# Kernel tuning notes

Measured on AMD Instinct MI355X. Metric: run time of the kernel, lower is better.

The kernel has to match this reference:

```python
import jax, jax.numpy as jnp
import numpy as np

E, D_IN, D_HID, D_OUT, B = 8, 128, 256, 128, 65536


def setup_inputs() -> dict:
    key = jax.random.key(0)
    ks = jax.random.split(key, 6)
    s1 = 1.0 / np.sqrt(D_IN)
    s2 = 1.0 / np.sqrt(D_HID)
    return {
        "x": jax.random.normal(ks[0], (B, D_IN), dtype=jnp.float32),
        "weights": jax.random.uniform(ks[1], (B, E), dtype=jnp.float32),
        "W1": jax.random.uniform(ks[2], (E, D_IN, D_HID), jnp.float32, -s1, s1),
        "b1": jax.random.uniform(ks[3], (E, D_HID), jnp.float32, -s1, s1),
        "W2": jax.random.uniform(ks[4], (E, D_HID, D_OUT), jnp.float32, -s2, s2),
        "b2": jax.random.uniform(ks[5], (E, D_OUT), jnp.float32, -s2, s2),
    }


def reference(x, weights, W1, b1, W2, b2):
    # all-experts dense MLP: every expert processes the full batch
    h = jax.nn.relu(jnp.einsum("bi,eih->beh", x, W1) + b1[None])  # [B,E,H]
    y = jnp.einsum("beh,eho->beo", h, W2) + b2[None]              # [B,E,O]
    # weighted combine over experts
    return jnp.einsum("beo,be->bo", y, weights)                   # [B,O]
```

## Files before the change

### kernel.cpp

```cpp
#include <hip/hip_runtime.h>


#define E_    8
#define DIN_  128
#define DH_   256
#define DOUT_ 128
#define BM_   128
#define NCHUNK 32
#define REC1  20480

typedef __attribute__((ext_vector_type(8))) short bf16x8;
typedef __attribute__((ext_vector_type(16))) float f32x16;
typedef __attribute__((ext_vector_type(2))) unsigned int uint2v;

__device__ __forceinline__ unsigned short f2bf(float f) {
  union { float f; unsigned int u; } v; v.f = f;
  unsigned int u = v.u;
  u += 0x7fffu + ((u >> 16) & 1u);
  return (unsigned short)(u >> 16);
}

__device__ __forceinline__ unsigned int cvt_pk_bf16(float lo, float hi) {
  unsigned int r;
  asm("v_cvt_pk_bf16_f32 %0, %1, %2" : "=v"(r) : "v"(lo), "v"(hi));
  return r;
}

__device__ __forceinline__ bf16x8 pack4(unsigned int a, unsigned int b,
                                        unsigned int c, unsigned int d) {
  union { unsigned int u[4]; bf16x8 v; } t;
  t.u[0] = a; t.u[1] = b; t.u[2] = c; t.u[3] = d;
  return t.v;
}

__device__ __forceinline__ void gload_lds16(const void* g, void* l) {
  __builtin_amdgcn_global_load_lds(
      (const __attribute__((address_space(1))) unsigned int*)g,
      (__attribute__((address_space(3))) unsigned int*)l, 16, 0, 0);
}

__global__ __launch_bounds__(256) void prep_w1(
    const float* __restrict__ W1, const float* __restrict__ b1,
    unsigned char* __restrict__ W1r)
{
  __shared__ float T[8192];
  const int t = blockIdx.x;
  const int e = t >> 2, hc = t & 3;
  const int tid = threadIdx.x;
  unsigned char* rec = W1r + (size_t)t * REC1;

  #pragma unroll
  for (int i = 0; i < 32; ++i) {
    int idx = i * 256 + tid;
    int k = idx >> 6, c = idx & 63;
    T[idx] = W1[((size_t)(e * DIN_ + k)) * DH_ + hc * 64 + c];
  }
  __syncthreads();
  #pragma unroll
  for (int j = 0; j < 16; ++j) {
    int widx = j * 256 + tid;
    int c = widx >> 6, uw = (widx & 63) * 4;
    int up = uw ^ ((c & 15) << 4);
    int k0 = up >> 1;
    unsigned int val = (unsigned int)f2bf(T[k0 * 64 + c]) |
                       ((unsigned int)f2bf(T[(k0 + 1) * 64 + c]) << 16);
    *(unsigned int*)(rec + c * 256 + uw) = val;
  }
  if (tid < 64) {
    *(unsigned int*)(rec + 16384 + tid * 32) =
        (unsigned int)f2bf(b1[e * DH_ + hc * 64 + tid]);
    #pragma unroll
    for (int p = 1; p < 8; ++p)
      *(unsigned int*)(rec + 16384 + tid * 32 + p * 4) = 0u;
  }
}

__global__ __launch_bounds__(256) void prep_w2p(
    const float* __restrict__ W2, unsigned int* __restrict__ W2p)
{
  const int t = blockIdx.x;
  const int e = t >> 2, hc = t & 3;
  const int tid = threadIdx.x;
  unsigned int* outw = W2p + (size_t)t * 4096;
  #pragma unroll
  for (int j = 0; j < 16; ++j) {
    int w = j * 256 + tid;
    int wh = w >> 11, k2 = (w >> 10) & 1, nf = (w >> 8) & 3;
    int lane = (w >> 2) & 63, pr = w & 3;
    int hi = lane >> 5, l32 = lane & 31;
    int n = nf * 32 + l32;
    int c = hc * 64 + wh * 32 + k2 * 16 + hi * 8 + pr * 2;
    unsigned int val =
        (unsigned int)f2bf(W2[((size_t)(e * DH_ + c)) * DOUT_ + n]) |
        ((unsigned int)f2bf(W2[((size_t)(e * DH_ + c + 1)) * DOUT_ + n]) << 16);
    outw[w] = val;
  }
}

__global__ __launch_bounds__(256, 2) void moe_main(
    const float* __restrict__ x, const float* __restrict__ wts,
    const float* __restrict__ b2, const unsigned char* __restrict__ W1r,
    const unsigned char* __restrict__ W2p, float* __restrict__ out)
{
  __shared__ __align__(16) unsigned char L[2][REC1];

  const int tid  = threadIdx.x;
  const int lane = tid & 63;
  const int wv   = tid >> 6;
  const int l32  = lane & 31;
  const int hi   = lane >> 5;
  const int swz4 = (l32 & 15) << 4;
  const long bm  = (long)blockIdx.x * BM_;
  const long m   = bm + wv * 32 + l32;

  auto stage = [&](int t, unsigned char* dst) {
    const unsigned char* src = W1r + (size_t)t * REC1;
    #pragma unroll
    for (int r = 0; r < 5; ++r)
      gload_lds16(src + (r * 256 + tid) * 16, dst + r * 4096 + wv * 1024);
  };

  stage(0, &L[0][0]);

  int p1o[8];
  #pragma unroll
  for (int ks = 0; ks < 8; ++ks)
    p1o[ks] = l32 * 256 + ((ks * 32 + hi * 16) ^ swz4);
  const int bo = 16384 + l32 * 32 + hi * 16;

  const bf16x8 ones = pack4(hi ? 0u : 0x3F80u, 0u, 0u, 0u);

  float wreg[8];
  {
    float4 a = *(const float4*)(wts + m * E_);
    float4 b = *(const float4*)(wts + m * E_ + 4);
    wreg[0] = a.x; wreg[1] = a.y; wreg[2] = a.z; wreg[3] = a.w;
    wreg[4] = b.x; wreg[5] = b.y; wreg[6] = b.z; wreg[7] = b.w;
  }

  bf16x8 xf[8];
  #pragma unroll
  for (int ks = 0; ks < 8; ++ks) {
    const float* xr = x + m * DIN_ + ks * 16 + hi * 8;
    float4 a = *(const float4*)xr;
    float4 b = *(const float4*)(xr + 4);
    xf[ks] = pack4(cvt_pk_bf16(a.x, a.y), cvt_pk_bf16(a.z, a.w),
                   cvt_pk_bf16(b.x, b.y), cvt_pk_bf16(b.z, b.w));
  }

  f32x16 oacc[4];
  #pragma unroll
  for (int nf = 0; nf < 4; ++nf) oacc[nf] = 0.0f;

  auto compute = [&](const unsigned char* Lb, int t, bf16x8* w2f) {
    const int e = t >> 2;
    const float w = wreg[e];
    bf16x8 bfr0 = *(const bf16x8*)(Lb + bo);
    bf16x8 bfr1 = *(const bf16x8*)(Lb + bo + 1024);

    f32x16 h0 = 0.0f, h1 = 0.0f;
    __builtin_amdgcn_s_setprio(1);
    #pragma unroll
    for (int ks = 0; ks < 8; ++ks) {
      bf16x8 a0 = *(const bf16x8*)(Lb + p1o[ks]);
      bf16x8 a1 = *(const bf16x8*)(Lb + p1o[ks] + 8192);
      h0 = __builtin_amdgcn_mfma_f32_32x32x16_bf16(a0, xf[ks], h0, 0, 0, 0);
      h1 = __builtin_amdgcn_mfma_f32_32x32x16_bf16(a1, xf[ks], h1, 0, 0, 0);
    }
    h0 = __builtin_amdgcn_mfma_f32_32x32x16_bf16(bfr0, ones, h0, 0, 0, 0);
    h1 = __builtin_amdgcn_mfma_f32_32x32x16_bf16(bfr1, ones, h1, 0, 0, 0);
    __builtin_amdgcn_s_setprio(0);

    bf16x8 hfr[4];
    #pragma unroll
    for (int cf = 0; cf < 2; ++cf) {
      const f32x16& hh = cf ? h1 : h0;
      unsigned int u[8];
      #pragma unroll
      for (int p = 0; p < 8; ++p) {
        float a = fmaxf(hh[2 * p],     0.0f) * w;
        float b = fmaxf(hh[2 * p + 1], 0.0f) * w;
        u[p] = cvt_pk_bf16(a, b);
      }
      uint2v s02 = __builtin_amdgcn_permlane32_swap(u[0], u[2], false, false);
      uint2v s13 = __builtin_amdgcn_permlane32_swap(u[1], u[3], false, false);
      uint2v s46 = __builtin_amdgcn_permlane32_swap(u[4], u[6], false, false);
      uint2v s57 = __builtin_amdgcn_permlane32_swap(u[5], u[7], false, false);
      hfr[2 * cf]     = pack4(s02[0], s13[0], s02[1], s13[1]);
      hfr[2 * cf + 1] = pack4(s46[0], s57[0], s46[1], s57[1]);
    }

    __builtin_amdgcn_s_setprio(1);
    #pragma unroll
    for (int kk = 0; kk < 4; ++kk) {
      #pragma unroll
      for (int nf = 0; nf < 4; ++nf) {
        bf16x8 b = w2f[(kk >> 1) * 8 + (kk & 1) * 4 + nf];
        oacc[nf] = __builtin_amdgcn_mfma_f32_32x32x16_bf16(hfr[kk], b, oacc[nf], 0, 0, 0);
      }
    }
    __builtin_amdgcn_s_setprio(0);
  };

  int cur = 0;
  for (int t = 0; t < NCHUNK; ++t) {
    __builtin_amdgcn_s_barrier();
    __builtin_amdgcn_sched_barrier(0);
    bf16x8 w2f[16];
    {
      const unsigned char* wb = W2p + (size_t)t * 16384 + lane * 16;
      #pragma unroll
      for (int i = 0; i < 16; ++i)
        w2f[i] = *(const bf16x8*)(wb + i * 1024);
    }
    if (t + 1 < NCHUNK) {
      stage(t + 1, &L[cur ^ 1][0]);
      __builtin_amdgcn_sched_barrier(0);
      asm volatile("s_waitcnt vmcnt(21)" ::: "memory");
    } else {
      __builtin_amdgcn_sched_barrier(0);
      asm volatile("s_waitcnt vmcnt(16)" ::: "memory");
    }
    __builtin_amdgcn_s_barrier();
    __builtin_amdgcn_sched_barrier(0);
    compute(&L[cur][0], t, w2f);
    cur ^= 1;
  }

  const unsigned int z = 0;
  bf16x8 wfrag = pack4(hi ? z : cvt_pk_bf16(wreg[0], wreg[1]),
                       hi ? z : cvt_pk_bf16(wreg[2], wreg[3]),
                       hi ? z : cvt_pk_bf16(wreg[4], wreg[5]),
                       hi ? z : cvt_pk_bf16(wreg[6], wreg[7]));
  #pragma unroll
  for (int nf = 0; nf < 4; ++nf) {
    const float* bp = b2 + nf * 32 + l32;
    bf16x8 bfrag = pack4(
        hi ? z : cvt_pk_bf16(bp[0 * DOUT_], bp[1 * DOUT_]),
        hi ? z : cvt_pk_bf16(bp[2 * DOUT_], bp[3 * DOUT_]),
        hi ? z : cvt_pk_bf16(bp[4 * DOUT_], bp[5 * DOUT_]),
        hi ? z : cvt_pk_bf16(bp[6 * DOUT_], bp[7 * DOUT_]));
    oacc[nf] = __builtin_amdgcn_mfma_f32_32x32x16_bf16(wfrag, bfrag, oacc[nf], 0, 0, 0);
  }

  #pragma unroll
  for (int nf = 0; nf < 4; ++nf) {
    #pragma unroll
    for (int r = 0; r < 16; ++r) {
      const int mloc = (r & 3) + 8 * (r >> 2) + 4 * hi;
      out[(bm + wv * 32 + mloc) * DOUT_ + nf * 32 + l32] = oacc[nf][r];
    }
  }
}

extern "C" void kernel_launch(void* const* d_in, const int* in_sizes, int n_in,
                              void* d_out, int out_size, void* d_ws, size_t ws_size,
                              hipStream_t stream) {
  const float* x   = (const float*)d_in[0];
  const float* wts = (const float*)d_in[1];
  const float* W1  = (const float*)d_in[2];
  const float* b1  = (const float*)d_in[3];
  const float* W2  = (const float*)d_in[4];
  const float* b2  = (const float*)d_in[5];
  float* out = (float*)d_out;

  unsigned char* W1r = (unsigned char*)d_ws;
  unsigned char* W2p = W1r + (size_t)NCHUNK * REC1;

  prep_w1<<<32, 256, 0, stream>>>(W1, b1, W1r);
  prep_w2p<<<32, 256, 0, stream>>>(W2, (unsigned int*)W2p);
  moe_main<<<65536 / BM_, 256, 0, stream>>>(x, wts, b2, W1r, W2p, out);
}
```

Baseline: 102.7 us.

## Use 512-thread blocks with staged LDS prefetch and split-phase MFMA schedule

```diff
diff --git a/kernel.cpp b/kernel.cpp
--- a/kernel.cpp
+++ b/kernel.cpp
@@ -5,9 +5,9 @@
 #define DIN_  128
 #define DH_   256
 #define DOUT_ 128
-#define BM_   128
+#define BM_   256
 #define NCHUNK 32
-#define REC1  20480
+#define REC1  18432
 
 typedef __attribute__((ext_vector_type(8))) short bf16x8;
 typedef __attribute__((ext_vector_type(16))) float f32x16;
@@ -97,7 +97,7 @@
   }
 }
 
-__global__ __launch_bounds__(256, 2) void moe_main(
+__global__ __launch_bounds__(512, 1) void moe_main(
     const float* __restrict__ x, const float* __restrict__ wts,
     const float* __restrict__ b2, const unsigned char* __restrict__ W1r,
     const unsigned char* __restrict__ W2p, float* __restrict__ out)
@@ -116,8 +116,10 @@
   auto stage = [&](int t, unsigned char* dst) {
     const unsigned char* src = W1r + (size_t)t * REC1;
     #pragma unroll
-    for (int r = 0; r < 5; ++r)
-      gload_lds16(src + (r * 256 + tid) * 16, dst + r * 4096 + wv * 1024);
+    for (int r = 0; r < 2; ++r)
+      gload_lds16(src + (r * 512 + tid) * 16, dst + r * 8192 + wv * 1024);
+    if (tid < 128)
+      gload_lds16(src + 16384 + tid * 16, dst + 16384 + wv * 1024);
   };
 
   stage(0, &L[0][0]);
@@ -152,25 +154,69 @@
   #pragma unroll
   for (int nf = 0; nf < 4; ++nf) oacc[nf] = 0.0f;
 
-  auto compute = [&](const unsigned char* Lb, int t, bf16x8* w2f) {
-    const int e = t >> 2;
-    const float w = wreg[e];
+  for (int t = 0; t < NCHUNK; ++t) {
+    const unsigned char* Lb = &L[t & 1][0];
+    unsigned char* Ln = &L[(t + 1) & 1][0];
+
+    bf16x8 w2f[16];
+    {
+      const unsigned char* wb = W2p + (size_t)t * 16384 + lane * 16;
+      #pragma unroll
+      for (int i = 0; i < 16; ++i)
+        w2f[i] = *(const bf16x8*)(wb + i * 1024);
+    }
+    __builtin_amdgcn_sched_barrier(0);
+    asm volatile("s_waitcnt vmcnt(16)" ::: "memory");
+    __builtin_amdgcn_sched_barrier(0);
+    __builtin_amdgcn_s_barrier();
+    __builtin_amdgcn_sched_barrier(0);
+
+    bf16x8 a0[4], a1[4];
+    #pragma unroll
+    for (int ks = 0; ks < 4; ++ks) {
+      a0[ks] = *(const bf16x8*)(Lb + p1o[ks]);
+      a1[ks] = *(const bf16x8*)(Lb + p1o[ks] + 8192);
+    }
     bf16x8 bfr0 = *(const bf16x8*)(Lb + bo);
     bf16x8 bfr1 = *(const bf16x8*)(Lb + bo + 1024);
+    if (t + 1 < NCHUNK) stage(t + 1, Ln);
+    __builtin_amdgcn_sched_barrier(0);
+    __builtin_amdgcn_s_barrier();
+    asm volatile("s_waitcnt lgkmcnt(0)" ::: "memory");
+    __builtin_amdgcn_sched_barrier(0);
 
     f32x16 h0 = 0.0f, h1 = 0.0f;
     __builtin_amdgcn_s_setprio(1);
-    #pragma unroll
-    for (int ks = 0; ks < 8; ++ks) {
-      bf16x8 a0 = *(const bf16x8*)(Lb + p1o[ks]);
-      bf16x8 a1 = *(const bf16x8*)(Lb + p1o[ks] + 8192);
-      h0 = __builtin_amdgcn_mfma_f32_32x32x16_bf16(a0, xf[ks], h0, 0, 0, 0);
-      h1 = __builtin_amdgcn_mfma_f32_32x32x16_bf16(a1, xf[ks], h1, 0, 0, 0);
-    }
     h0 = __builtin_amdgcn_mfma_f32_32x32x16_bf16(bfr0, ones, h0, 0, 0, 0);
     h1 = __builtin_amdgcn_mfma_f32_32x32x16_bf16(bfr1, ones, h1, 0, 0, 0);
+    #pragma unroll
+    for (int ks = 0; ks < 4; ++ks) {
+      h0 = __builtin_amdgcn_mfma_f32_32x32x16_bf16(a0[ks], xf[ks], h0, 0, 0, 0);
+      h1 = __builtin_amdgcn_mfma_f32_32x32x16_bf16(a1[ks], xf[ks], h1, 0, 0, 0);
+    }
     __builtin_amdgcn_s_setprio(0);
-
+    __builtin_amdgcn_sched_barrier(0);
+
+    bf16x8 b0[4], b1v[4];
+    #pragma unroll
+    for (int ks = 0; ks < 4; ++ks) {
+      b0[ks] = *(const bf16x8*)(Lb + p1o[ks + 4]);
+      b1v[ks] = *(const bf16x8*)(Lb + p1o[ks + 4] + 8192);
+    }
+    __builtin_amdgcn_sched_barrier(0);
+    __builtin_amdgcn_s_barrier();
+    asm volatile("s_waitcnt lgkmcnt(0)" ::: "memory");
+    __builtin_amdgcn_sched_barrier(0);
+    __builtin_amdgcn_s_setprio(1);
+    #pragma unroll
+    for (int ks = 0; ks < 4; ++ks) {
+      h0 = __builtin_amdgcn_mfma_f32_32x32x16_bf16(b0[ks], xf[ks + 4], h0, 0, 0, 0);
+      h1 = __builtin_amdgcn_mfma_f32_32x32x16_bf16(b1v[ks], xf[ks + 4], h1, 0, 0, 0);
+    }
+    __builtin_amdgcn_s_setprio(0);
+    __builtin_amdgcn_sched_barrier(0);
+
+    const float w = wreg[t >> 2];
     bf16x8 hfr[4];
     #pragma unroll
     for (int cf = 0; cf < 2; ++cf) {
@@ -189,7 +235,12 @@
       hfr[2 * cf]     = pack4(s02[0], s13[0], s02[1], s13[1]);
       hfr[2 * cf + 1] = pack4(s46[0], s57[0], s46[1], s57[1]);
     }
-
+    if (t + 1 < NCHUNK) {
+      asm volatile("s_waitcnt vmcnt(2)" ::: "memory");
+    } else {
+      asm volatile("s_waitcnt vmcnt(0)" ::: "memory");
+    }
+    __builtin_amdgcn_sched_barrier(0);
     __builtin_amdgcn_s_setprio(1);
     #pragma unroll
     for (int kk = 0; kk < 4; ++kk) {
@@ -200,31 +251,7 @@
       }
     }
     __builtin_amdgcn_s_setprio(0);
-  };
-
-  int cur = 0;
-  for (int t = 0; t < NCHUNK; ++t) {
-    __builtin_amdgcn_s_barrier();
-    __builtin_amdgcn_sched_barrier(0);
-    bf16x8 w2f[16];
-    {
-      const unsigned char* wb = W2p + (size_t)t * 16384 + lane * 16;
-      #pragma unroll
-      for (int i = 0; i < 16; ++i)
-        w2f[i] = *(const bf16x8*)(wb + i * 1024);
-    }
-    if (t + 1 < NCHUNK) {
-      stage(t + 1, &L[cur ^ 1][0]);
-      __builtin_amdgcn_sched_barrier(0);
-      asm volatile("s_waitcnt vmcnt(21)" ::: "memory");
-    } else {
-      __builtin_amdgcn_sched_barrier(0);
-      asm volatile("s_waitcnt vmcnt(16)" ::: "memory");
-    }
-    __builtin_amdgcn_s_barrier();
-    __builtin_amdgcn_sched_barrier(0);
-    compute(&L[cur][0], t, w2f);
-    cur ^= 1;
+    __builtin_amdgcn_sched_barrier(0);
   }
 
   const unsigned int z = 0;
@@ -269,5 +296,5 @@
 
   prep_w1<<<32, 256, 0, stream>>>(W1, b1, W1r);
   prep_w2p<<<32, 256, 0, stream>>>(W2, (unsigned int*)W2p);
-  moe_main<<<65536 / BM_, 256, 0, stream>>>(x, wts, b2, W1r, W2p, out);
-}
+  moe_main<<<65536 / BM_, 512, 0, stream>>>(x, wts, b2, W1r, W2p, out);
+}
```

Result: faster. 98.99 us (-3.6%).

## Software-pipeline GEMM1 of next chunk with GEMM2 of current chunk

Applied to the files above, without the earlier changes.

```diff
diff --git a/kernel.cpp b/kernel.cpp
--- a/kernel.cpp
+++ b/kernel.cpp
@@ -12,6 +12,9 @@
 typedef __attribute__((ext_vector_type(8))) short bf16x8;
 typedef __attribute__((ext_vector_type(16))) float f32x16;
 typedef __attribute__((ext_vector_type(2))) unsigned int uint2v;
+
+#define MFMA32 __builtin_amdgcn_mfma_f32_32x32x16_bf16
+#define SB()   __builtin_amdgcn_sched_barrier(0)
 
 __device__ __forceinline__ unsigned short f2bf(float f) {
   union { float f; unsigned int u; } v; v.f = f;
@@ -120,14 +123,11 @@
       gload_lds16(src + (r * 256 + tid) * 16, dst + r * 4096 + wv * 1024);
   };
 
-  stage(0, &L[0][0]);
-
   int p1o[8];
   #pragma unroll
   for (int ks = 0; ks < 8; ++ks)
     p1o[ks] = l32 * 256 + ((ks * 32 + hi * 16) ^ swz4);
   const int bo = 16384 + l32 * 32 + hi * 16;
-
   const bf16x8 ones = pack4(hi ? 0u : 0x3F80u, 0u, 0u, 0u);
 
   float wreg[8];
@@ -137,7 +137,6 @@
     wreg[0] = a.x; wreg[1] = a.y; wreg[2] = a.z; wreg[3] = a.w;
     wreg[4] = b.x; wreg[5] = b.y; wreg[6] = b.z; wreg[7] = b.w;
   }
-
   bf16x8 xf[8];
   #pragma unroll
   for (int ks = 0; ks < 8; ++ks) {
@@ -147,31 +146,20 @@
     xf[ks] = pack4(cvt_pk_bf16(a.x, a.y), cvt_pk_bf16(a.z, a.w),
                    cvt_pk_bf16(b.x, b.y), cvt_pk_bf16(b.z, b.w));
   }
+  stage(0, &L[0][0]);
+  SB();
+  asm volatile("s_waitcnt vmcnt(0)" ::: "memory");
+  SB();
+  __builtin_amdgcn_s_barrier();
+  SB();
 
   f32x16 oacc[4];
   #pragma unroll
   for (int nf = 0; nf < 4; ++nf) oacc[nf] = 0.0f;
 
-  auto compute = [&](const unsigned char* Lb, int t, bf16x8* w2f) {
-    const int e = t >> 2;
-    const float w = wreg[e];
-    bf16x8 bfr0 = *(const bf16x8*)(Lb + bo);
-    bf16x8 bfr1 = *(const bf16x8*)(Lb + bo + 1024);
-
-    f32x16 h0 = 0.0f, h1 = 0.0f;
-    __builtin_amdgcn_s_setprio(1);
-    #pragma unroll
-    for (int ks = 0; ks < 8; ++ks) {
-      bf16x8 a0 = *(const bf16x8*)(Lb + p1o[ks]);
-      bf16x8 a1 = *(const bf16x8*)(Lb + p1o[ks] + 8192);
-      h0 = __builtin_amdgcn_mfma_f32_32x32x16_bf16(a0, xf[ks], h0, 0, 0, 0);
-      h1 = __builtin_amdgcn_mfma_f32_32x32x16_bf16(a1, xf[ks], h1, 0, 0, 0);
-    }
-    h0 = __builtin_amdgcn_mfma_f32_32x32x16_bf16(bfr0, ones, h0, 0, 0, 0);
-    h1 = __builtin_amdgcn_mfma_f32_32x32x16_bf16(bfr1, ones, h1, 0, 0, 0);
-    __builtin_amdgcn_s_setprio(0);
-
-    bf16x8 hfr[4];
+  bf16x8 hfr[4];
+
+  auto repack = [&](const f32x16& h0, const f32x16& h1, float w) {
     #pragma unroll
     for (int cf = 0; cf < 2; ++cf) {
       const f32x16& hh = cf ? h1 : h0;
@@ -189,42 +177,127 @@
       hfr[2 * cf]     = pack4(s02[0], s13[0], s02[1], s13[1]);
       hfr[2 * cf + 1] = pack4(s46[0], s57[0], s46[1], s57[1]);
     }
+  };
+
+  {
+    const unsigned char* Lb = &L[0][0];
+    bf16x8 a0[8], a1[8];
+    #pragma unroll
+    for (int ks = 0; ks < 8; ++ks) {
+      a0[ks] = *(const bf16x8*)(Lb + p1o[ks]);
+      a1[ks] = *(const bf16x8*)(Lb + p1o[ks] + 8192);
+    }
+    bf16x8 bfr0 = *(const bf16x8*)(Lb + bo);
+    bf16x8 bfr1 = *(const bf16x8*)(Lb + bo + 1024);
+    stage(1, &L[1][0]);
+    SB();
+    asm volatile("s_waitcnt lgkmcnt(0)" ::: "memory");
+    SB();
+    f32x16 h0 = 0.0f, h1 = 0.0f;
+    h0 = MFMA32(bfr0, ones, h0, 0, 0, 0);
+    h1 = MFMA32(bfr1, ones, h1, 0, 0, 0);
+    #pragma unroll
+    for (int ks = 0; ks < 8; ++ks) {
+      h0 = MFMA32(a0[ks], xf[ks], h0, 0, 0, 0);
+      h1 = MFMA32(a1[ks], xf[ks], h1, 0, 0, 0);
+    }
+    repack(h0, h1, wreg[0]);
+  }
+
+  for (int t = 0; t < NCHUNK; ++t) {
+    const bool hn = (t + 1 < NCHUNK);
+    const bool hs = (t + 2 < NCHUNK);
+    const unsigned char* Lb = &L[(t + 1) & 1][0];
+    unsigned char* Ld = &L[t & 1][0];
+    const unsigned char* wb = W2p + (size_t)t * 16384 + lane * 16;
+
+    SB();
+    asm volatile("s_waitcnt vmcnt(0)" ::: "memory");
+    SB();
+    __builtin_amdgcn_s_barrier();
+    SB();
+
+    f32x16 h0 = 0.0f, h1 = 0.0f;
+
+    bf16x8 w2fA[8];
+    #pragma unroll
+    for (int i = 0; i < 8; ++i) w2fA[i] = *(const bf16x8*)(wb + i * 1024);
+    bf16x8 a0[4], a1[4], bfr0, bfr1;
+    if (hn) {
+      #pragma unroll
+      for (int ks = 0; ks < 4; ++ks) {
+        a0[ks] = *(const bf16x8*)(Lb + p1o[ks]);
+        a1[ks] = *(const bf16x8*)(Lb + p1o[ks] + 8192);
+      }
+      bfr0 = *(const bf16x8*)(Lb + bo);
+      bfr1 = *(const bf16x8*)(Lb + bo + 1024);
+    }
+    SB();
+    asm volatile("s_waitcnt lgkmcnt(0)" ::: "memory");
+    asm volatile("s_waitcnt vmcnt(0)" ::: "memory");
+    SB();
 
     __builtin_amdgcn_s_setprio(1);
-    #pragma unroll
-    for (int kk = 0; kk < 4; ++kk) {
+    oacc[0] = MFMA32(hfr[0], w2fA[0], oacc[0], 0, 0, 0);
+    oacc[1] = MFMA32(hfr[0], w2fA[1], oacc[1], 0, 0, 0);
+    if (hn) { h0 = MFMA32(bfr0, ones, h0, 0, 0, 0);
+              h1 = MFMA32(bfr1, ones, h1, 0, 0, 0); }
+    oacc[2] = MFMA32(hfr[0], w2fA[2], oacc[2], 0, 0, 0);
+    oacc[3] = MFMA32(hfr[0], w2fA[3], oacc[3], 0, 0, 0);
+    if (hn) { h0 = MFMA32(a0[0], xf[0], h0, 0, 0, 0);
+              h1 = MFMA32(a1[0], xf[0], h1, 0, 0, 0); }
+    oacc[0] = MFMA32(hfr[1], w2fA[4], oacc[0], 0, 0, 0);
+    oacc[1] = MFMA32(hfr[1], w2fA[5], oacc[1], 0, 0, 0);
+    if (hn) { h0 = MFMA32(a0[1], xf[1], h0, 0, 0, 0);
+              h1 = MFMA32(a1[1], xf[1], h1, 0, 0, 0); }
+    oacc[2] = MFMA32(hfr[1], w2fA[6], oacc[2], 0, 0, 0);
+    oacc[3] = MFMA32(hfr[1], w2fA[7], oacc[3], 0, 0, 0);
+    if (hn) { h0 = MFMA32(a0[2], xf[2], h0, 0, 0, 0);
+              h1 = MFMA32(a1[2], xf[2], h1, 0, 0, 0);
+              h0 = MFMA32(a0[3], xf[3], h0, 0, 0, 0);
+              h1 = MFMA32(a1[3], xf[3], h1, 0, 0, 0); }
+    __builtin_amdgcn_s_setprio(0);
+    SB();
+
+    bf16x8 w2fB[8];
+    #pragma unroll
+    for (int i = 0; i < 8; ++i) w2fB[i] = *(const bf16x8*)(wb + (8 + i) * 1024);
+    bf16x8 b0[4], b1v[4];
+    if (hn) {
       #pragma unroll
-      for (int nf = 0; nf < 4; ++nf) {
-        bf16x8 b = w2f[(kk >> 1) * 8 + (kk & 1) * 4 + nf];
-        oacc[nf] = __builtin_amdgcn_mfma_f32_32x32x16_bf16(hfr[kk], b, oacc[nf], 0, 0, 0);
+      for (int ks = 0; ks < 4; ++ks) {
+        b0[ks]  = *(const bf16x8*)(Lb + p1o[ks + 4]);
+        b1v[ks] = *(const bf16x8*)(Lb + p1o[ks + 4] + 8192);
       }
     }
+    if (hs) stage(t + 2, Ld);
+    SB();
+    asm volatile("s_waitcnt lgkmcnt(0)" ::: "memory");
+    if (hs) { asm volatile("s_waitcnt vmcnt(5)" ::: "memory"); }
+    else    { asm volatile("s_waitcnt vmcnt(0)" ::: "memory"); }
+    SB();
+
+    __builtin_amdgcn_s_setprio(1);
+    oacc[0] = MFMA32(hfr[2], w2fB[0], oacc[0], 0, 0, 0);
+    oacc[1] = MFMA32(hfr[2], w2fB[1], oacc[1], 0, 0, 0);
+    if (hn) { h0 = MFMA32(b0[0], xf[4], h0, 0, 0, 0);
+              h1 = MFMA32(b1v[0], xf[4], h1, 0, 0, 0); }
+    oacc[2] = MFMA32(hfr[2], w2fB[2], oacc[2], 0, 0, 0);
+    oacc[3] = MFMA32(hfr[2], w2fB[3], oacc[3], 0, 0, 0);
+    if (hn) { h0 = MFMA32(b0[1], xf[5], h0, 0, 0, 0);
+              h1 = MFMA32(b1v[1], xf[5], h1, 0, 0, 0); }
+    oacc[0] = MFMA32(hfr[3], w2fB[4], oacc[0], 0, 0, 0);
+    oacc[1] = MFMA32(hfr[3], w2fB[5], oacc[1], 0, 0, 0);
+    if (hn) { h0 = MFMA32(b0[2], xf[6], h0, 0, 0, 0);
+              h1 = MFMA32(b1v[2], xf[6], h1, 0, 0, 0); }
+    oacc[2] = MFMA32(hfr[3], w2fB[6], oacc[2], 0, 0, 0);
+    oacc[3] = MFMA32(hfr[3], w2fB[7], oacc[3], 0, 0, 0);
+    if (hn) { h0 = MFMA32(b0[3], xf[7], h0, 0, 0, 0);
+              h1 = MFMA32(b1v[3], xf[7], h1, 0, 0, 0); }
     __builtin_amdgcn_s_setprio(0);
-  };
-
-  int cur = 0;
-  for (int t = 0; t < NCHUNK; ++t) {
-    __builtin_amdgcn_s_barrier();
-    __builtin_amdgcn_sched_barrier(0);
-    bf16x8 w2f[16];
-    {
-      const unsigned char* wb = W2p + (size_t)t * 16384 + lane * 16;
-      #pragma unroll
-      for (int i = 0; i < 16; ++i)
-        w2f[i] = *(const bf16x8*)(wb + i * 1024);
-    }
-    if (t + 1 < NCHUNK) {
-      stage(t + 1, &L[cur ^ 1][0]);
-      __builtin_amdgcn_sched_barrier(0);
-      asm volatile("s_waitcnt vmcnt(21)" ::: "memory");
-    } else {
-      __builtin_amdgcn_sched_barrier(0);
-      asm volatile("s_waitcnt vmcnt(16)" ::: "memory");
-    }
-    __builtin_amdgcn_s_barrier();
-    __builtin_amdgcn_sched_barrier(0);
-    compute(&L[cur][0], t, w2f);
-    cur ^= 1;
+    SB();
+
+    if (hn) repack(h0, h1, wreg[(t + 1) >> 2]);
   }
 
   const unsigned int z = 0;
@@ -240,7 +313,7 @@
         hi ? z : cvt_pk_bf16(bp[2 * DOUT_], bp[3 * DOUT_]),
         hi ? z : cvt_pk_bf16(bp[4 * DOUT_], bp[5 * DOUT_]),
         hi ? z : cvt_pk_bf16(bp[6 * DOUT_], bp[7 * DOUT_]));
-    oacc[nf] = __builtin_amdgcn_mfma_f32_32x32x16_bf16(wfrag, bfrag, oacc[nf], 0, 0, 0);
+    oacc[nf] = MFMA32(wfrag, bfrag, oacc[nf], 0, 0, 0);
   }
 
   #pragma unroll
```

Measured after the change: 106.4 us. 3.5% more time.
